# Kernel tuning notes

Hardware: AMD Instinct MI355X
Metric: run time of the kernel (lower is better)

Reference implementation:

```python
import jax, jax.numpy as jnp
import numpy as np

N_NODES = 100000
N_EDGES = 1600000
D_IN = 128
D_HID = 128
D_OUT = 64
DROP_P = 0.5


def setup_inputs() -> dict:
    key = jax.random.key(0)
    ks = jax.random.split(key, 8)
    x = jax.random.normal(ks[0], (N_NODES, D_IN), dtype=jnp.float32)
    edge_index = jax.random.randint(ks[1], (2, N_EDGES), 0, N_NODES, dtype=jnp.int64)
    s = lambda fi, fo: 1.0 / np.sqrt(fi)
    W1_l = jax.random.uniform(ks[2], (D_IN, D_HID), jnp.float32, -s(D_IN, D_HID), s(D_IN, D_HID))
    W1_r = jax.random.uniform(ks[3], (D_IN, D_HID), jnp.float32, -s(D_IN, D_HID), s(D_IN, D_HID))
    b1 = jnp.zeros((D_HID,), jnp.float32)
    W2_l = jax.random.uniform(ks[4], (D_HID, D_OUT), jnp.float32, -s(D_HID, D_OUT), s(D_HID, D_OUT))
    W2_r = jax.random.uniform(ks[5], (D_HID, D_OUT), jnp.float32, -s(D_HID, D_OUT), s(D_HID, D_OUT))
    b2 = jnp.zeros((D_OUT,), jnp.float32)
    return {"x": x, "edge_index": edge_index, "W1_l": W1_l, "b1": b1, "W1_r": W1_r,
            "W2_l": W2_l, "b2": b2, "W2_r": W2_r}


def reference(x, edge_index, W1_l, b1, W1_r, W2_l, b2, W2_r):
    N = x.shape[0]
    src = edge_index[0]  # message source x_j
    dst = edge_index[1]  # aggregation target x_i
    # in-degree for mean aggregation (clamped to avoid div-by-zero)
    deg = jax.ops.segment_sum(jnp.ones((src.shape[0],), x.dtype), dst, num_segments=N)
    inv_deg = (1.0 / jnp.maximum(deg, 1.0))[:, None]  # [N,1]

    def sage(h, Wl, b, Wr):
        # mean over incoming neighbors, then lin_l(agg) + bias + lin_r(root)
        agg = jax.ops.segment_sum(h[src], dst, num_segments=N) * inv_deg  # [N,F]
        return agg @ Wl + b + h @ Wr

    h = jax.nn.relu(sage(x, W1_l, b1, W1_r))
    # dropout p=0.5 (training mode), deterministic key
    keep = jax.random.bernoulli(jax.random.key(42), 1.0 - DROP_P, h.shape)
    h = jnp.where(keep, h / (1.0 - DROP_P), 0.0)
    out = sage(h, W2_l, b2, W2_r)
    return jax.nn.log_softmax(out, axis=-1)
```

## Files before the change

### kernel.cpp

```cpp
#include <hip/hip_runtime.h>
#include <stdint.h>

#define D_FEAT 128
#define D_OUT  64
#define BSH 7
#define MAXB 1024
#define BCAP 4096
#define H1P  136
#define SCAT_BLKS 512

typedef __attribute__((ext_vector_type(8))) short short8;
typedef __attribute__((ext_vector_type(8))) ushort ushort8;
typedef __attribute__((ext_vector_type(4))) float f32x4;
typedef __attribute__((ext_vector_type(2))) float f32x2;

__device__ __forceinline__ ushort f2bf(float f) {
  uint32_t u = __float_as_uint(f);
  return (ushort)((u + 0x7FFFu + ((u >> 16) & 1u)) >> 16);
}
__device__ __forceinline__ float bf2f(ushort v) {
  return __uint_as_float((uint32_t)v << 16);
}
__device__ __forceinline__ void acc2(f32x2& a, uint32_t w) {
  f32x2 t;
  t.x = __uint_as_float(w << 16);
  t.y = __uint_as_float(w);
  a += t;
}
__device__ __forceinline__ void accq(f32x2& a, f32x2& b, uint32_t w) {
  a += __builtin_amdgcn_cvt_pk_f32_fp8(w, false);
  b += __builtin_amdgcn_cvt_pk_f32_fp8(w, true);
}

__device__ __forceinline__ void threefry2x32(uint32_t k0, uint32_t k1,
                                             uint32_t& x0, uint32_t& x1) {
  uint32_t k2 = k0 ^ k1 ^ 0x1BD11BDAu;
#define TF_ROT(r) { x0 += x1; x1 = (x1 << (r)) | (x1 >> (32 - (r))); x1 ^= x0; }
  x0 += k0; x1 += k1;
  TF_ROT(13) TF_ROT(15) TF_ROT(26) TF_ROT(6)
  x0 += k1; x1 += k2 + 1u;
  TF_ROT(17) TF_ROT(29) TF_ROT(16) TF_ROT(24)
  x0 += k2; x1 += k0 + 2u;
  TF_ROT(13) TF_ROT(15) TF_ROT(26) TF_ROT(6)
  x0 += k0; x1 += k1 + 3u;
  TF_ROT(17) TF_ROT(29) TF_ROT(16) TF_ROT(24)
  x0 += k1; x1 += k2 + 4u;
  TF_ROT(13) TF_ROT(15) TF_ROT(26) TF_ROT(6)
  x0 += k2; x1 += k0 + 5u;
#undef TF_ROT
}

__device__ __forceinline__ bool keep_bit(uint32_t i) {
  uint32_t t0 = 0u, t1 = i;
  threefry2x32(0u, 42u, t0, t1);
  return (((t0 ^ t1) >> 31) == 0u);
}

__device__ __forceinline__ int load_dst(const void* ei, int is64, long E, long e) {
  return is64 ? (int)((const long long*)ei)[E + e] : ((const int*)ei)[E + e];
}
__device__ __forceinline__ int load_src(const void* ei, int is64, long E, long e) {
  return is64 ? (int)((const long long*)ei)[e] : ((const int*)ei)[e];
}

__global__ __launch_bounds__(256) void prep_kernel(
    const float4* __restrict__ x, const void* __restrict__ ei,
    ushort* __restrict__ xb, uint8_t* __restrict__ xq,
    const float* __restrict__ W1l, const float* __restrict__ W1r,
    const float* __restrict__ W2l, const float* __restrict__ W2r,
    ushort* __restrict__ w1t, ushort* __restrict__ w2lt, ushort* __restrict__ w2rt,
    ushort* __restrict__ y2, int* __restrict__ bucketOff,
    uint32_t* __restrict__ packed,
    long E, long n4, int N, int nbuck, int chunkE, int nConv) {
  const int b = blockIdx.x;
  const int tid = threadIdx.x;

  if (b < SCAT_BLKS) {
    __shared__ int cnt[MAXB];
    __shared__ int base[MAXB];
    __shared__ int cur[MAXB];
    __shared__ int is64_s;
    if (tid < 64) {
      uint32_t v = ((const uint32_t*)ei)[2 * tid + 1];
      unsigned long long nz = __ballot(v != 0u);
      if (tid == 0) is64_s = (nz == 0ull) ? 1 : 0;
    }
    for (int i = tid; i < nbuck; i += 256) { cnt[i] = 0; cur[i] = 0; }
    __syncthreads();
    const int is64 = is64_s;
    long beg = (long)b * chunkE;
    long end = beg + chunkE; if (end > E) end = E;
    for (long e = beg + tid; e < end; e += 256)
      atomicAdd(&cnt[load_dst(ei, is64, E, e) >> BSH], 1);
    __syncthreads();
    for (int i = tid; i < nbuck; i += 256)
      base[i] = cnt[i] ? atomicAdd(&bucketOff[i], cnt[i]) : 0;
    __syncthreads();
    for (long e = beg + tid; e < end; e += 256) {
      int dst = load_dst(ei, is64, E, e);
      int src = load_src(ei, is64, E, e);
      int bk = dst >> BSH;
      int off = atomicAdd(&cur[bk], 1);
      packed[(long)bk * BCAP + base[bk] + off] =
          ((uint32_t)src << BSH) | (uint32_t)(dst & ((1 << BSH) - 1));
    }
  } else if (b < SCAT_BLKS + nConv) {
    long i = (long)(b - SCAT_BLKS) * 256 + tid;
    if (i < n4) {
      float4 v = x[i];
      ushort4 o = {f2bf(v.x), f2bf(v.y), f2bf(v.z), f2bf(v.w)};
      *(ushort4*)(xb + i * 4) = o;
      int p = 0;
      p = __builtin_amdgcn_cvt_pk_fp8_f32(v.x, v.y, p, false);
      p = __builtin_amdgcn_cvt_pk_fp8_f32(v.z, v.w, p, true);
      ((uint32_t*)xq)[i] = (uint32_t)p;
    }
  } else if (b < SCAT_BLKS + nConv + 128) {
    int idx = (b - SCAT_BLKS - nConv) * 256 + tid;
    int j = idx >> 8, k = idx & 255;
    float v = (k < 128) ? W1l[k * 128 + j] : W1r[(k - 128) * 128 + j];
    w1t[j * 256 + k] = f2bf(v);
  } else if (b < SCAT_BLKS + nConv + 128 + 32) {
    int idx = (b - SCAT_BLKS - nConv - 128) * 256 + tid;
    int j = idx >> 7, k = idx & 127;
    w2lt[j * 128 + k] = f2bf(W2l[k * 64 + j]);
  } else if (b < SCAT_BLKS + nConv + 128 + 64) {
    int idx = (b - SCAT_BLKS - nConv - 160) * 256 + tid;
    int j = idx >> 7, k = idx & 127;
    w2rt[j * 128 + k] = f2bf(W2r[k * 64 + j]);
  } else {
    if (tid < 16)
      *(ushort8*)(xb + (long)N * D_FEAT + tid * 8) = (ushort8){0,0,0,0,0,0,0,0};
    else if (tid < 24)
      *(uint4*)(xq + (long)N * D_FEAT + (tid - 16) * 16) = (uint4){0,0,0,0};
    else if (tid < 32)
      *(ushort8*)(y2 + (long)N * D_OUT + (tid - 24) * 8) = (ushort8){0,0,0,0,0,0,0,0};
  }
}

__global__ __launch_bounds__(256) void bucket_build(
    uint32_t* __restrict__ packed, const int* __restrict__ bucketOff,
    int* __restrict__ rowptr, int* __restrict__ rowend,
    float* __restrict__ invd, int N) {
  __shared__ uint32_t sp[BCAP];
  __shared__ int lcnt[1 << BSH];
  __shared__ int lbase[1 << BSH];
  __shared__ int lcur[1 << BSH];
  const int b = blockIdx.x;
  const int tid = threadIdx.x;
  const int beg = b * BCAP;
  const int cnt = bucketOff[b];
  for (int i = tid; i < cnt; i += 256) sp[i] = packed[beg + i];
  if (tid < 128) { lcnt[tid] = 0; lcur[tid] = 0; }
  __syncthreads();
  for (int i = tid; i < cnt; i += 256)
    atomicAdd(&lcnt[sp[i] & 127], 1);
  __syncthreads();
  if (tid < 128) lbase[tid] = lcnt[tid];
  __syncthreads();
  for (int off = 1; off < 128; off <<= 1) {
    int t = (tid >= off && tid < 128) ? lbase[tid - off] : 0;
    __syncthreads();
    if (tid < 128) lbase[tid] += t;
    __syncthreads();
  }
  if (tid < 128) {
    int excl = lbase[tid] - lcnt[tid];
    lbase[tid] = excl;
    int n = (b << BSH) + tid;
    if (n < N) {
      rowptr[n] = beg + excl;
      rowend[n] = beg + excl + lcnt[tid];
      int d = lcnt[tid];
      invd[n] = 1.0f / (float)(d > 1 ? d : 1);
    }
  }
  __syncthreads();
  for (int i = tid; i < cnt; i += 256) {
    uint32_t p = sp[i];
    int l = p & 127;
    int pos = beg + lbase[l] + atomicAdd(&lcur[l], 1);
    packed[pos] = p >> BSH;
  }
}

__global__ __launch_bounds__(256) void agg_kernel(
    const uint8_t* __restrict__ xq, const int* __restrict__ rowptr,
    const int* __restrict__ rowend, const int* __restrict__ col,
    const float* __restrict__ invd, ushort* __restrict__ aggb,
    unsigned long long* __restrict__ maskb, int N) {
  const int lane = threadIdx.x & 63;
  const int q  = lane >> 4;
  const int sl = lane & 15;
  const uint32_t slb = (uint32_t)sl * 8u;
  int n = (int)(((long)blockIdx.x * blockDim.x + threadIdx.x) >> 6);
  if (n >= N) return;

  if (maskb) {
    uint32_t base = (uint32_t)n * 128u;
    bool k0 = keep_bit(base + (uint32_t)lane);
    bool k1 = keep_bit(base + 64u + (uint32_t)lane);
    unsigned long long w0 = __ballot(k0);
    unsigned long long w1 = __ballot(k1);
    if (lane == 0) {
      maskb[2 * n]     = w0;
      maskb[2 * n + 1] = w1;
    }
  }

  const char* xc = (const char*)xq;
  const int beg = rowptr[n], end = rowend[n];
  const uint32_t zoff = ((uint32_t)N << 7) + slb;

  f32x2 acc[4];
#pragma unroll
  for (int i = 0; i < 4; i++) acc[i] = (f32x2){0.f, 0.f};

  for (int e = beg + q; e < end; e += 16) {
    int c0 = col[e], c1 = col[e + 4], c2 = col[e + 8], c3 = col[e + 12];
    uint32_t o0 = ((uint32_t)c0 << 7) + slb;
    uint32_t o1 = (e + 4  < end) ? (((uint32_t)c1 << 7) + slb) : zoff;
    uint32_t o2 = (e + 8  < end) ? (((uint32_t)c2 << 7) + slb) : zoff;
    uint32_t o3 = (e + 12 < end) ? (((uint32_t)c3 << 7) + slb) : zoff;
    uint2 a = *(const uint2*)(xc + o0);
    uint2 b = *(const uint2*)(xc + o1);
    uint2 c = *(const uint2*)(xc + o2);
    uint2 d = *(const uint2*)(xc + o3);
    accq(acc[0], acc[1], a.x); accq(acc[2], acc[3], a.y);
    accq(acc[0], acc[1], b.x); accq(acc[2], acc[3], b.y);
    accq(acc[0], acc[1], c.x); accq(acc[2], acc[3], c.y);
    accq(acc[0], acc[1], d.x); accq(acc[2], acc[3], d.y);
  }

#pragma unroll
  for (int i = 0; i < 4; i++) {
    acc[i].x += __shfl_xor(acc[i].x, 16);
    acc[i].y += __shfl_xor(acc[i].y, 16);
    acc[i].x += __shfl_xor(acc[i].x, 32);
    acc[i].y += __shfl_xor(acc[i].y, 32);
  }

  if (q == 0) {
    float sc = invd[n];
    ushort8 o;
#pragma unroll
    for (int i = 0; i < 4; i++) {
      o[2 * i]     = f2bf(acc[i].x * sc);
      o[2 * i + 1] = f2bf(acc[i].y * sc);
    }
    *(ushort8*)(aggb + (long)n * D_FEAT + sl * 8) = o;
  }
}

__global__ __launch_bounds__(256) void fused12_kernel(
    const ushort* __restrict__ aggb, const ushort* __restrict__ xb,
    const ushort* __restrict__ w1t, const float* __restrict__ b1,
    const unsigned long long* __restrict__ maskb,
    const ushort* __restrict__ w2lt, const ushort* __restrict__ w2rt,
    const float* __restrict__ b2,
    ushort* __restrict__ y2, ushort* __restrict__ z, int N) {
  __shared__ __align__(16) ushort smem[33792];
  ushort* w1s = smem;
  ushort* h1s = smem;
  ushort* wsl = smem + 17408;
  ushort* wsr = smem + 25600;

  const int tid = threadIdx.x;
  const int lane = tid & 63;
  const int wv = tid >> 6;
  const int r16 = lane & 15;
  const int kg = lane >> 4;

  {
    const uint32_t swz = ((uint32_t)(tid >> 5) & 7u) << 4;
#pragma unroll
    for (int i = 0; i < 16; i++) {
      uint32_t byte = (uint32_t)i * 4096u + (uint32_t)tid * 16u;
      uint4 v = *(const uint4*)((const char*)w1t + byte);
      *(uint4*)((char*)w1s + (byte ^ swz)) = v;
    }
  }
  __syncthreads();

  const int node_base = blockIdx.x * 128 + wv * 32;
  int ar0 = node_base + r16;       if (ar0 >= N) ar0 = N - 1;
  int ar1 = node_base + 16 + r16;  if (ar1 >= N) ar1 = N - 1;

  f32x4 acc0[8], acc1[8];
#pragma unroll
  for (int i = 0; i < 8; i++) {
    acc0[i] = (f32x4){0.f, 0.f, 0.f, 0.f};
    acc1[i] = (f32x4){0.f, 0.f, 0.f, 0.f};
  }

  {
    const ushort* a0g = aggb + (long)ar0 * 128 + kg * 8;
    const ushort* a0x = xb   + (long)ar0 * 128 + kg * 8;
    const ushort* a1g = aggb + (long)ar1 * 128 + kg * 8;
    const ushort* a1x = xb   + (long)ar1 * 128 + kg * 8;
    const uint32_t rswz = ((uint32_t)(r16 & 7)) << 4;
#pragma unroll
    for (int s = 0; s < 8; s++) {
      short8 aT0 = (s < 4) ? *(const short8*)(a0g + s * 32)
                           : *(const short8*)(a0x + (s - 4) * 32);
      short8 aT1 = (s < 4) ? *(const short8*)(a1g + s * 32)
                           : *(const short8*)(a1x + (s - 4) * 32);
#pragma unroll
      for (int ct = 0; ct < 8; ct++) {
        uint32_t boff = ((uint32_t)(ct * 16 + r16) * 512u +
                         (uint32_t)s * 64u + (uint32_t)kg * 16u) ^ rswz;
        short8 b = *(const short8*)((const char*)w1s + boff);
        acc0[ct] = __builtin_amdgcn_mfma_f32_16x16x32_bf16(aT0, b, acc0[ct], 0, 0, 0);
        acc1[ct] = __builtin_amdgcn_mfma_f32_16x16x32_bf16(aT1, b, acc1[ct], 0, 0, 0);
      }
    }
  }
  __syncthreads();

  {
    const uint32_t swz = ((uint32_t)(tid >> 4) & 7u) << 4;
#pragma unroll
    for (int i = 0; i < 4; i++) {
      uint32_t byte = (uint32_t)i * 4096u + (uint32_t)tid * 16u;
      uint4 vl = *(const uint4*)((const char*)w2lt + byte);
      uint4 vr = *(const uint4*)((const char*)w2rt + byte);
      *(uint4*)((char*)wsl + (byte ^ swz)) = vl;
      *(uint4*)((char*)wsr + (byte ^ swz)) = vr;
    }
  }

  {
    float bbv[8];
#pragma unroll
    for (int ct = 0; ct < 8; ct++) bbv[ct] = b1[ct * 16 + r16];
#pragma unroll
    for (int t = 0; t < 2; t++) {
      const f32x4* acc = t ? acc1 : acc0;
#pragma unroll
      for (int r = 0; r < 4; r++) {
        int row_l = wv * 32 + t * 16 + kg * 4 + r;
        int n = blockIdx.x * 128 + row_l;
        int mi = (n < N) ? n : (N - 1);
        unsigned long long m0 = maskb[2 * mi];
        unsigned long long m1 = maskb[2 * mi + 1];
        ushort* dst = h1s + row_l * H1P + r16;
#pragma unroll
        for (int ct = 0; ct < 8; ct++) {
          int j = ct * 16 + r16;
          float h = fmaxf(acc[ct][r] + bbv[ct], 0.f);
          unsigned long long w = (j & 64) ? m1 : m0;
          bool keep = (w >> (j & 63)) & 1ull;
          dst[ct * 16] = keep ? f2bf(2.0f * h) : (ushort)0;
        }
      }
    }
  }
  __syncthreads();

  f32x4 aL[2][4], aR[2][4];
#pragma unroll
  for (int t = 0; t < 2; t++)
#pragma unroll
    for (int i = 0; i < 4; i++) {
      aL[t][i] = (f32x4){0.f, 0.f, 0.f, 0.f};
      aR[t][i] = (f32x4){0.f, 0.f, 0.f, 0.f};
    }

  {
    const uint32_t rswz = ((uint32_t)(r16 & 7)) << 4;
#pragma unroll
    for (int s = 0; s < 4; s++) {
#pragma unroll
      for (int t = 0; t < 2; t++) {
        const ushort* ap = h1s + (wv * 32 + t * 16 + r16) * H1P + s * 32 + kg * 8;
        short8 a = *(const short8*)ap;
#pragma unroll
        for (int ct = 0; ct < 4; ct++) {
          uint32_t boff = ((uint32_t)(ct * 16 + r16) * 256u +
                           (uint32_t)s * 64u + (uint32_t)kg * 16u) ^ rswz;
          short8 bl = *(const short8*)((const char*)wsl + boff);
          short8 br = *(const short8*)((const char*)wsr + boff);
          aL[t][ct] = __builtin_amdgcn_mfma_f32_16x16x32_bf16(a, bl, aL[t][ct], 0, 0, 0);
          aR[t][ct] = __builtin_amdgcn_mfma_f32_16x16x32_bf16(a, br, aR[t][ct], 0, 0, 0);
        }
      }
    }
  }

  float bb[4];
#pragma unroll
  for (int ct = 0; ct < 4; ct++) bb[ct] = b2[ct * 16 + r16];

#pragma unroll
  for (int t = 0; t < 2; t++) {
    int nb = node_base + t * 16;
#pragma unroll
    for (int r = 0; r < 4; r++) {
      int n = nb + kg * 4 + r;
      if (n < N) {
#pragma unroll
        for (int ct = 0; ct < 4; ct++) {
          y2[(long)n * D_OUT + ct * 16 + r16] = f2bf(aL[t][ct][r]);
          z [(long)n * D_OUT + ct * 16 + r16] = f2bf(aR[t][ct][r] + bb[ct]);
        }
      }
    }
  }
}

__global__ __launch_bounds__(256) void agg64_kernel(
    const ushort* __restrict__ y2, const ushort* __restrict__ z,
    const int* __restrict__ rowptr, const int* __restrict__ rowend,
    const int* __restrict__ col, const float* __restrict__ invd,
    float* __restrict__ out, int N) {
  const int lane = threadIdx.x & 63;
  const int g  = lane >> 3;
  const int sl = lane & 7;
  const uint32_t slb = (uint32_t)sl * 16u;
  int n = (int)(((long)blockIdx.x * blockDim.x + threadIdx.x) >> 6);
  if (n >= N) return;

  const char* xc = (const char*)y2;
  const int beg = rowptr[n], end = rowend[n];
  const uint32_t zoff = ((uint32_t)N << 7) + slb;

  f32x2 acc[4];
#pragma unroll
  for (int i = 0; i < 4; i++) acc[i] = (f32x2){0.f, 0.f};

  for (int e = beg + g; e < end; e += 16) {
    int c0 = col[e], c1 = col[e + 8];
    uint32_t o0 = ((uint32_t)c0 << 7) + slb;
    uint32_t o1 = (e + 8 < end) ? (((uint32_t)c1 << 7) + slb) : zoff;
    uint4 a = *(const uint4*)(xc + o0);
    uint4 b = *(const uint4*)(xc + o1);
    acc2(acc[0], a.x); acc2(acc[1], a.y); acc2(acc[2], a.z); acc2(acc[3], a.w);
    acc2(acc[0], b.x); acc2(acc[1], b.y); acc2(acc[2], b.z); acc2(acc[3], b.w);
  }

#pragma unroll
  for (int i = 0; i < 4; i++) {
    acc[i].x += __shfl_xor(acc[i].x, 8);
    acc[i].y += __shfl_xor(acc[i].y, 8);
    acc[i].x += __shfl_xor(acc[i].x, 16);
    acc[i].y += __shfl_xor(acc[i].y, 16);
    acc[i].x += __shfl_xor(acc[i].x, 32);
    acc[i].y += __shfl_xor(acc[i].y, 32);
  }

  if (g == 0) {
    float sc = invd[n];
    ushort8 zr = *(const ushort8*)(z + (long)n * D_OUT + sl * 8);
    float v[8];
#pragma unroll
    for (int i = 0; i < 4; i++) {
      v[2 * i]     = acc[i].x * sc + bf2f(zr[2 * i]);
      v[2 * i + 1] = acc[i].y * sc + bf2f(zr[2 * i + 1]);
    }
    float m = v[0];
#pragma unroll
    for (int j = 1; j < 8; j++) m = fmaxf(m, v[j]);
    m = fmaxf(m, __shfl_xor(m, 1));
    m = fmaxf(m, __shfl_xor(m, 2));
    m = fmaxf(m, __shfl_xor(m, 4));
    float s = 0.f;
#pragma unroll
    for (int j = 0; j < 8; j++) s += expf(v[j] - m);
    s += __shfl_xor(s, 1);
    s += __shfl_xor(s, 2);
    s += __shfl_xor(s, 4);
    float ls = m + logf(s);
    float4 o0 = {v[0] - ls, v[1] - ls, v[2] - ls, v[3] - ls};
    float4 o1 = {v[4] - ls, v[5] - ls, v[6] - ls, v[7] - ls};
    float* op = out + (long)n * D_OUT + sl * 8;
    *(float4*)op = o0;
    *(float4*)(op + 4) = o1;
  }
}

extern "C" void kernel_launch(void* const* d_in, const int* in_sizes, int n_in,
                              void* d_out, int out_size, void* d_ws, size_t ws_size,
                              hipStream_t stream) {
  const float* x   = (const float*)d_in[0];
  const void*  ei  = d_in[1];
  const float* W1l = (const float*)d_in[2];
  const float* b1  = (const float*)d_in[3];
  const float* W1r = (const float*)d_in[4];
  const float* W2l = (const float*)d_in[5];
  const float* b2  = (const float*)d_in[6];
  const float* W2r = (const float*)d_in[7];
  float* out = (float*)d_out;

  const int  N  = in_sizes[0] / D_FEAT;
  const long E  = (long)in_sizes[1] / 2;
  const long NF = (long)N * D_FEAT;
  const int  nbuck = (N + (1 << BSH) - 1) >> BSH;

  char* ws = (char*)d_ws;
  size_t off = 0;
  auto alloc = [&](size_t bytes) -> void* {
    void* p = ws + off;
    off = (off + bytes + 255) & ~(size_t)255;
    return p;
  };
  int*      bucketOff = (int*)alloc(sizeof(int) * MAXB);
  int*      rowptr    = (int*)alloc(sizeof(int) * N);
  int*      rowend    = (int*)alloc(sizeof(int) * N);
  uint32_t* packed    = (uint32_t*)alloc(sizeof(uint32_t) * ((size_t)nbuck * BCAP + 16));
  float*    invd      = (float*)alloc(sizeof(float) * N);
  ushort*   xb        = (ushort*)alloc(sizeof(ushort) * (NF + D_FEAT));
  uint8_t*  xq        = (uint8_t*)alloc(sizeof(uint8_t) * (NF + D_FEAT));
  ushort*   aggb      = (ushort*)alloc(sizeof(ushort) * NF);
  ushort*   yz        = (ushort*)alloc(sizeof(ushort) * (NF + 512));
  ushort*   w1t       = (ushort*)alloc(sizeof(ushort) * 128 * 256);
  ushort*   w2lt      = (ushort*)alloc(sizeof(ushort) * 64 * 128);
  ushort*   w2rt      = (ushort*)alloc(sizeof(ushort) * 64 * 128);
  unsigned long long* maskb = (unsigned long long*)alloc(sizeof(unsigned long long) * 2 * N);

  int* col = (int*)packed;
  ushort* y2 = yz;
  ushort* z  = yz + ((size_t)N * D_OUT + 256);

  const long n4 = NF / 4;
  const int nConv = (int)((n4 + 255) / 256);
  const int chunkE = (int)((E + SCAT_BLKS - 1) / SCAT_BLKS);
  const int prepBlocks = SCAT_BLKS + nConv + 128 + 64 + 1;

  hipMemsetAsync(bucketOff, 0, sizeof(int) * MAXB, stream);

  prep_kernel<<<prepBlocks, 256, 0, stream>>>(
      (const float4*)x, ei, xb, xq, W1l, W1r, W2l, W2r,
      w1t, w2lt, w2rt, y2, bucketOff, packed,
      E, n4, N, nbuck, chunkE, nConv);

  bucket_build<<<nbuck, 256, 0, stream>>>(packed, bucketOff, rowptr, rowend, invd, N);

  const int aggBlocks = (int)(((long)N * 64 + 255) / 256);
  const int gemmBlocks = (N + 127) / 128;

  agg_kernel<<<aggBlocks, 256, 0, stream>>>(xq, rowptr, rowend, col, invd, aggb, maskb, N);
  fused12_kernel<<<gemmBlocks, 256, 0, stream>>>(aggb, xb, w1t, b1, maskb,
                                                 w2lt, w2rt, b2, y2, z, N);
  agg64_kernel<<<aggBlocks, 256, 0, stream>>>(y2, z, rowptr, rowend, col, invd, out, N);
}
```

Baseline: 185.7 us.

## Store layer-2 messages as fp8 and compute dropout mask inside fused GEMM

The layer-2 left projection y2 is now stored as 8-bit fp8 (reusing the xq buffer), so the second gather reads 64 bytes per neighbor instead of 128. The agg64 kernel now decodes fp8 with accq. Dropout mask generation moves from agg_kernel into fused12_kernel shared memory, which removes the maskb global buffer and its traffic. This adds fp8 quantization error to the layer-2 aggregation and extra threefry work inside the GEMM kernel.

```diff
diff --git a/kernel.cpp b/kernel.cpp
--- a/kernel.cpp
+++ b/kernel.cpp
@@ -69,8 +69,7 @@
     const float* __restrict__ W1l, const float* __restrict__ W1r,
     const float* __restrict__ W2l, const float* __restrict__ W2r,
     ushort* __restrict__ w1t, ushort* __restrict__ w2lt, ushort* __restrict__ w2rt,
-    ushort* __restrict__ y2, int* __restrict__ bucketOff,
-    uint32_t* __restrict__ packed,
+    int* __restrict__ bucketOff, uint32_t* __restrict__ packed,
     long E, long n4, int N, int nbuck, int chunkE, int nConv) {
   const int b = blockIdx.x;
   const int tid = threadIdx.x;
@@ -133,8 +132,6 @@
       *(ushort8*)(xb + (long)N * D_FEAT + tid * 8) = (ushort8){0,0,0,0,0,0,0,0};
     else if (tid < 24)
       *(uint4*)(xq + (long)N * D_FEAT + (tid - 16) * 16) = (uint4){0,0,0,0};
-    else if (tid < 32)
-      *(ushort8*)(y2 + (long)N * D_OUT + (tid - 24) * 8) = (ushort8){0,0,0,0,0,0,0,0};
   }
 }
 
@@ -187,26 +184,13 @@
 __global__ __launch_bounds__(256) void agg_kernel(
     const uint8_t* __restrict__ xq, const int* __restrict__ rowptr,
     const int* __restrict__ rowend, const int* __restrict__ col,
-    const float* __restrict__ invd, ushort* __restrict__ aggb,
-    unsigned long long* __restrict__ maskb, int N) {
+    const float* __restrict__ invd, ushort* __restrict__ aggb, int N) {
   const int lane = threadIdx.x & 63;
   const int q  = lane >> 4;
   const int sl = lane & 15;
   const uint32_t slb = (uint32_t)sl * 8u;
   int n = (int)(((long)blockIdx.x * blockDim.x + threadIdx.x) >> 6);
   if (n >= N) return;
-
-  if (maskb) {
-    uint32_t base = (uint32_t)n * 128u;
-    bool k0 = keep_bit(base + (uint32_t)lane);
-    bool k1 = keep_bit(base + 64u + (uint32_t)lane);
-    unsigned long long w0 = __ballot(k0);
-    unsigned long long w1 = __ballot(k1);
-    if (lane == 0) {
-      maskb[2 * n]     = w0;
-      maskb[2 * n + 1] = w1;
-    }
-  }
 
   const char* xc = (const char*)xq;
   const int beg = rowptr[n], end = rowend[n];
@@ -255,11 +239,11 @@
 __global__ __launch_bounds__(256) void fused12_kernel(
     const ushort* __restrict__ aggb, const ushort* __restrict__ xb,
     const ushort* __restrict__ w1t, const float* __restrict__ b1,
-    const unsigned long long* __restrict__ maskb,
     const ushort* __restrict__ w2lt, const ushort* __restrict__ w2rt,
     const float* __restrict__ b2,
-    ushort* __restrict__ y2, ushort* __restrict__ z, int N) {
+    uint8_t* __restrict__ y2q, ushort* __restrict__ z, int N) {
   __shared__ __align__(16) ushort smem[33792];
+  __shared__ unsigned long long mask_s[128][2];
   ushort* w1s = smem;
   ushort* h1s = smem;
   ushort* wsl = smem + 17408;
@@ -271,6 +255,9 @@
   const int r16 = lane & 15;
   const int kg = lane >> 4;
 
+  if (blockIdx.x == 0 && tid < 4)
+    ((uint4*)(y2q + (long)N * D_OUT))[tid] = (uint4){0, 0, 0, 0};
+
   {
     const uint32_t swz = ((uint32_t)(tid >> 5) & 7u) << 4;
 #pragma unroll
@@ -278,6 +265,20 @@
       uint32_t byte = (uint32_t)i * 4096u + (uint32_t)tid * 16u;
       uint4 v = *(const uint4*)((const char*)w1t + byte);
       *(uint4*)((char*)w1s + (byte ^ swz)) = v;
+    }
+  }
+
+  {
+    const int nb0 = blockIdx.x * 128 + wv * 32;
+#pragma unroll 2
+    for (int w = 0; w < 64; ++w) {
+      int nl = w >> 1;
+      int word = w & 1;
+      int n = nb0 + nl;
+      int mi = (n < N) ? n : (N - 1);
+      bool kb = keep_bit((uint32_t)mi * 128u + (uint32_t)word * 64u + (uint32_t)lane);
+      unsigned long long bm = __ballot(kb);
+      if (lane == 0) mask_s[wv * 32 + nl][word] = bm;
     }
   }
   __syncthreads();
@@ -339,10 +340,8 @@
 #pragma unroll
       for (int r = 0; r < 4; r++) {
         int row_l = wv * 32 + t * 16 + kg * 4 + r;
-        int n = blockIdx.x * 128 + row_l;
-        int mi = (n < N) ? n : (N - 1);
-        unsigned long long m0 = maskb[2 * mi];
-        unsigned long long m1 = maskb[2 * mi + 1];
+        unsigned long long m0 = mask_s[row_l][0];
+        unsigned long long m1 = mask_s[row_l][1];
         ushort* dst = h1s + row_l * H1P + r16;
 #pragma unroll
         for (int ct = 0; ct < 8; ct++) {
@@ -400,8 +399,10 @@
       if (n < N) {
 #pragma unroll
         for (int ct = 0; ct < 4; ct++) {
-          y2[(long)n * D_OUT + ct * 16 + r16] = f2bf(aL[t][ct][r]);
-          z [(long)n * D_OUT + ct * 16 + r16] = f2bf(aR[t][ct][r] + bb[ct]);
+          float yv = aL[t][ct][r];
+          int p = __builtin_amdgcn_cvt_pk_fp8_f32(yv, yv, 0, false);
+          y2q[(long)n * D_OUT + ct * 16 + r16] = (uint8_t)p;
+          z  [(long)n * D_OUT + ct * 16 + r16] = f2bf(aR[t][ct][r] + bb[ct]);
         }
       }
     }
@@ -409,20 +410,20 @@
 }
 
 __global__ __launch_bounds__(256) void agg64_kernel(
-    const ushort* __restrict__ y2, const ushort* __restrict__ z,
+    const uint8_t* __restrict__ y2q, const ushort* __restrict__ z,
     const int* __restrict__ rowptr, const int* __restrict__ rowend,
     const int* __restrict__ col, const float* __restrict__ invd,
     float* __restrict__ out, int N) {
   const int lane = threadIdx.x & 63;
   const int g  = lane >> 3;
   const int sl = lane & 7;
-  const uint32_t slb = (uint32_t)sl * 16u;
+  const uint32_t slb = (uint32_t)sl * 8u;
   int n = (int)(((long)blockIdx.x * blockDim.x + threadIdx.x) >> 6);
   if (n >= N) return;
 
-  const char* xc = (const char*)y2;
+  const char* xc = (const char*)y2q;
   const int beg = rowptr[n], end = rowend[n];
-  const uint32_t zoff = ((uint32_t)N << 7) + slb;
+  const uint32_t zoff = ((uint32_t)N << 6) + slb;
 
   f32x2 acc[4];
 #pragma unroll
@@ -430,12 +431,12 @@
 
   for (int e = beg + g; e < end; e += 16) {
     int c0 = col[e], c1 = col[e + 8];
-    uint32_t o0 = ((uint32_t)c0 << 7) + slb;
-    uint32_t o1 = (e + 8 < end) ? (((uint32_t)c1 << 7) + slb) : zoff;
-    uint4 a = *(const uint4*)(xc + o0);
-    uint4 b = *(const uint4*)(xc + o1);
-    acc2(acc[0], a.x); acc2(acc[1], a.y); acc2(acc[2], a.z); acc2(acc[3], a.w);
-    acc2(acc[0], b.x); acc2(acc[1], b.y); acc2(acc[2], b.z); acc2(acc[3], b.w);
+    uint32_t o0 = ((uint32_t)c0 << 6) + slb;
+    uint32_t o1 = (e + 8 < end) ? (((uint32_t)c1 << 6) + slb) : zoff;
+    uint2 a = *(const uint2*)(xc + o0);
+    uint2 b = *(const uint2*)(xc + o1);
+    accq(acc[0], acc[1], a.x); accq(acc[2], acc[3], a.y);
+    accq(acc[0], acc[1], b.x); accq(acc[2], acc[3], b.y);
   }
 
 #pragma unroll
@@ -511,15 +512,13 @@
   ushort*   xb        = (ushort*)alloc(sizeof(ushort) * (NF + D_FEAT));
   uint8_t*  xq        = (uint8_t*)alloc(sizeof(uint8_t) * (NF + D_FEAT));
   ushort*   aggb      = (ushort*)alloc(sizeof(ushort) * NF);
-  ushort*   yz        = (ushort*)alloc(sizeof(ushort) * (NF + 512));
+  ushort*   z         = (ushort*)alloc(sizeof(ushort) * ((size_t)N * D_OUT + 256));
   ushort*   w1t       = (ushort*)alloc(sizeof(ushort) * 128 * 256);
   ushort*   w2lt      = (ushort*)alloc(sizeof(ushort) * 64 * 128);
   ushort*   w2rt      = (ushort*)alloc(sizeof(ushort) * 64 * 128);
-  unsigned long long* maskb = (unsigned long long*)alloc(sizeof(unsigned long long) * 2 * N);
 
   int* col = (int*)packed;
-  ushort* y2 = yz;
-  ushort* z  = yz + ((size_t)N * D_OUT + 256);
+  uint8_t* y2q = xq;
 
   const long n4 = NF / 4;
   const int nConv = (int)((n4 + 255) / 256);
@@ -530,7 +529,7 @@
 
   prep_kernel<<<prepBlocks, 256, 0, stream>>>(
       (const float4*)x, ei, xb, xq, W1l, W1r, W2l, W2r,
-      w1t, w2lt, w2rt, y2, bucketOff, packed,
+      w1t, w2lt, w2rt, bucketOff, packed,
       E, n4, N, nbuck, chunkE, nConv);
 
   bucket_build<<<nbuck, 256, 0, stream>>>(packed, bucketOff, rowptr, rowend, invd, N);
@@ -538,8 +537,8 @@
   const int aggBlocks = (int)(((long)N * 64 + 255) / 256);
   const int gemmBlocks = (N + 127) / 128;
 
-  agg_kernel<<<aggBlocks, 256, 0, stream>>>(xq, rowptr, rowend, col, invd, aggb, maskb, N);
-  fused12_kernel<<<gemmBlocks, 256, 0, stream>>>(aggb, xb, w1t, b1, maskb,
-                                                 w2lt, w2rt, b2, y2, z, N);
-  agg64_kernel<<<aggBlocks, 256, 0, stream>>>(y2, z, rowptr, rowend, col, invd, out, N);
-}
+  agg_kernel<<<aggBlocks, 256, 0, stream>>>(xq, rowptr, rowend, col, invd, aggb, N);
+  fused12_kernel<<<gemmBlocks, 256, 0, stream>>>(aggb, xb, w1t, b1,
+                                                 w2lt, w2rt, b2, y2q, z, N);
+  agg64_kernel<<<aggBlocks, 256, 0, stream>>>(y2q, z, rowptr, rowend, col, invd, out, N);
+}
```

New measurement: 200.6 us. 1.08x slower.
